# Performance work log

Measured on AMD Instinct MI355X. Metric: run time of the kernel, lower is better.

Reference implementation:

```python
import jax, jax.numpy as jnp
import numpy as np
from jax import lax

BS = 131072
L = 128          # pitch dim (conv input length)
NUM_CH = 10
EMB = 256
Z_DIM = 128
K = 64           # num codebook embeddings
COMMIT = 0.25


def setup_inputs() -> dict:
    key = jax.random.key(0)
    ks = jax.random.split(key, 10)
    pr = jax.random.uniform(ks[0], (BS, L), dtype=jnp.float32)
    track_pad_mask = jax.random.randint(ks[1], (BS,), 0, 2).astype(jnp.bool_)
    conv_w = jax.random.normal(ks[2], (NUM_CH, 1, 12), dtype=jnp.float32) * 0.1
    conv_b = jnp.zeros((NUM_CH,), jnp.float32)
    fc_w = jax.random.normal(ks[3], (EMB, NUM_CH * 29), dtype=jnp.float32) * 0.05
    fc_b = jnp.zeros((EMB,), jnp.float32)
    mu_w = jax.random.normal(ks[4], (Z_DIM, EMB), dtype=jnp.float32) * 0.05
    mu_b = jnp.zeros((Z_DIM,), jnp.float32)
    codebook = jax.random.normal(ks[5], (K, Z_DIM), dtype=jnp.float32)
    return {"pr": pr, "track_pad_mask": track_pad_mask, "conv_w": conv_w,
            "conv_b": conv_b, "fc_w": fc_w, "fc_b": fc_b,
            "mu_w": mu_w, "mu_b": mu_b, "codebook": codebook}


def _encode(pr, conv_w, conv_b, fc_w, fc_b, mu_w, mu_b):
    # Conv1d(1 -> NUM_CH, k=12, stride=1, VALID): [bs,1,128] -> [bs,10,117]
    x = lax.conv_general_dilated(pr[:, None, :], conv_w, (1,), 'VALID',
                                 dimension_numbers=('NCH', 'OIH', 'NCH'))
    x = jax.nn.relu(x + conv_b[None, :, None])
    # MaxPool1d(4,4): [bs,10,117] -> [bs,10,29]
    x = lax.reduce_window(x, -jnp.inf, lax.max, (1, 1, 4), (1, 1, 4), 'VALID')
    x = x.reshape(x.shape[0], -1)               # [bs, 290]
    x = x @ fc_w.T + fc_b                       # [bs, 256]
    mu = x @ mu_w.T + mu_b                      # [bs, 128]
    return mu


def _vq(mu, codebook, track_pad_mask):
    # squared L2 distances [bs, K]
    d = (jnp.sum(mu * mu, axis=1, keepdims=True)
         - 2.0 * mu @ codebook.T
         + jnp.sum(codebook * codebook, axis=1)[None, :])
    idx = jnp.argmin(d, axis=1)                 # [bs]
    q = codebook[idx]                           # gather [bs, Z_DIM]
    valid = (~track_pad_mask).astype(mu.dtype)  # [bs]
    n_valid = jnp.maximum(jnp.sum(valid), 1.0)
    # commitment loss over non-padded rows
    e_latent = jnp.sum(((lax.stop_gradient(q) - mu) ** 2) * valid[:, None]) / (n_valid * mu.shape[1])
    cmt_loss = COMMIT * e_latent
    # straight-through estimator
    z = mu + lax.stop_gradient(q - mu)
    # perplexity over non-padded assignments
    counts = jnp.zeros((K,), mu.dtype).at[idx].add(valid)
    probs = counts / n_valid
    perplexity = jnp.exp(-jnp.sum(probs * jnp.log(probs + 1e-10)))
    return z, cmt_loss, perplexity


def reference(pr, track_pad_mask, conv_w, conv_b, fc_w, fc_b, mu_w, mu_b, codebook):
    mu = _encode(pr, conv_w, conv_b, fc_w, fc_b, mu_w, mu_b)
    z, cmt_loss, perplexity = _vq(mu, codebook, track_pad_mask)
    return z, cmt_loss, perplexity
```

## Files before the change

kernel.cpp:

```cpp
#include <hip/hip_runtime.h>
#include <math.h>

#define BS 131072
#define L 128
#define NCH 10
#define EMB 256
#define ZD 128
#define KCB 64
#define NF 290
#define RPB 64
#define TPB 128

typedef __attribute__((ext_vector_type(8))) short short8;
typedef __attribute__((ext_vector_type(4))) float float4v;

#define WS_BC    0
#define WS_CNORM 128
#define WS_CBT   192
#define WS_CNT   8384
#define WS_ESUM  8448
#define WS_WHI   8452
#define WS_WLO   28932

static __device__ __forceinline__ short f2bf(float x) {
  unsigned u = __float_as_uint(x);
  return (short)((u + 0x7fffu + ((u >> 16) & 1u)) >> 16);
}
static __device__ __forceinline__ float bf2f(short s) {
  return __uint_as_float(((unsigned)(unsigned short)s) << 16);
}

__global__ void k_prep(const float* __restrict__ fc_w, const float* __restrict__ fc_b,
                       const float* __restrict__ mu_w, const float* __restrict__ mu_b,
                       const float* __restrict__ codebook, float* __restrict__ ws) {
  const int b = blockIdx.x, t = threadIdx.x;
  if (b < 80) {
    __shared__ float fcT[32 * 260];
    __shared__ float mus[16 * 260];
    const int c = b >> 4, ks = (b >> 3) & 1, nt = b & 7;
    const int f0 = c * 58 + ks * 32;

    {
      const int kk = t & 31, esub = t >> 5;
      const bool valid = (ks * 32 + kk) < 58;
#pragma unroll
      for (int p = 0; p < 32; ++p) {
        int e = p * 8 + esub;
        fcT[kk * 260 + e] = valid ? fc_w[e * NF + f0 + kk] : 0.0f;
      }
    }
    {
#pragma unroll
      for (int p = 0; p < 4; ++p) {
        int idx = p * 256 + t;
        int zz = idx >> 6, e4 = idx & 63;
        *(float4*)&mus[zz * 260 + e4 * 4] =
            *(const float4*)&mu_w[(nt * 16 + zz) * EMB + e4 * 4];
      }
    }
    __syncthreads();

    const int lane_lo = t >> 3, j = t & 7;
    const int z = lane_lo & 15;
    const int kka = ((lane_lo >> 4) & 1) * 8 + j;
    const int kkb = kka + 16;
    float a0 = 0, a1 = 0, a2 = 0, a3 = 0, b0 = 0, b1 = 0, b2 = 0, b3 = 0;
#pragma unroll 8
    for (int e = 0; e < 256; e += 4) {
      float4 m  = *(const float4*)&mus[z * 260 + e];
      float4 fa = *(const float4*)&fcT[kka * 260 + e];
      float4 fb = *(const float4*)&fcT[kkb * 260 + e];
      a0 = fmaf(m.x, fa.x, a0); a1 = fmaf(m.y, fa.y, a1);
      a2 = fmaf(m.z, fa.z, a2); a3 = fmaf(m.w, fa.w, a3);
      b0 = fmaf(m.x, fb.x, b0); b1 = fmaf(m.y, fb.y, b1);
      b2 = fmaf(m.z, fb.z, b2); b3 = fmaf(m.w, fb.w, b3);
    }
    float va = (a0 + a1) + (a2 + a3);
    float vb = (b0 + b1) + (b2 + b3);
    short* hi = (short*)(ws + WS_WHI);
    short* lo = (short*)(ws + WS_WLO);
    const int base = b * 512;
    short ha = f2bf(va); short la = f2bf(va - bf2f(ha));
    short hb = f2bf(vb); short lb = f2bf(vb - bf2f(hb));
    hi[base + t] = ha;        lo[base + t] = la;
    hi[base + 256 + t] = hb;  lo[base + 256 + t] = lb;
  } else if (b == 80) {
    if (t < ZD) {
      float p0 = 0, p1 = 0, p2 = 0, p3 = 0;
      const float* mw = mu_w + (size_t)t * EMB;
      for (int e = 0; e < EMB; e += 4) {
        p0 = fmaf(mw[e + 0], fc_b[e + 0], p0);
        p1 = fmaf(mw[e + 1], fc_b[e + 1], p1);
        p2 = fmaf(mw[e + 2], fc_b[e + 2], p2);
        p3 = fmaf(mw[e + 3], fc_b[e + 3], p3);
      }
      ws[WS_BC + t] = mu_b[t] + ((p0 + p1) + (p2 + p3));
    }
  } else if (b == 81) {
    if (t < KCB) {
      double acc = 0.0;
      for (int k = 0; k < ZD; ++k) { double v = (double)codebook[t * ZD + k]; acc += v * v; }
      ws[WS_CNORM + t] = (float)acc;
    } else if (t < 128) {
      ((int*)ws)[WS_CNT + (t - 64)] = 0;
    } else if (t == 128) {
      ws[WS_ESUM] = 0.0f;
    }
  } else {
    for (int i = 0; i < 32; ++i) {
      int idx = i * 256 + t;
      int k = idx >> 6, cc = idx & 63;
      ws[WS_CBT + idx] = codebook[cc * ZD + k];
    }
  }
}

__launch_bounds__(TPB, 2)
__global__ void k_main(const float* __restrict__ pr, const int* __restrict__ mask,
                       const float* __restrict__ conv_w, const float* __restrict__ conv_b,
                       const float* __restrict__ codebook,
                       float* __restrict__ ws, float* __restrict__ out) {
  __shared__ __align__(16) unsigned char lds_raw[33024];
  __shared__ float aux_val[RPB * 8];
  __shared__ int   aux_idx[RPB * 8];
  __shared__ int   bi_s[RPB];
  __shared__ float validf[RPB];
  __shared__ int   hist[KCB];

  short* feat_hi = (short*)lds_raw;
  short* feat_lo = (short*)(lds_raw + 9216);
  float* mu_s    = (float*)lds_raw;

  const int tid = threadIdx.x;
  const int lane = tid & 63, wv = tid >> 6;
  const int q4 = lane >> 4, c16 = lane & 15;
  const long rowg0 = (long)blockIdx.x * RPB;

  if (tid < KCB) hist[tid] = 0;
  for (int i = tid; i < RPB * 6; i += TPB) {
    int r = i / 6, kk = 58 + (i % 6);
    feat_hi[r * 72 + kk] = 0;
    feat_lo[r * 72 + kk] = 0;
  }

  const float* bc = ws + WS_BC;
  float4v acc[4][4];
#pragma unroll
  for (int ntl = 0; ntl < 4; ++ntl) {
    float bv = bc[wv * 64 + ntl * 16 + c16];
    float4v b4 = {bv, bv, bv, bv};
#pragma unroll
    for (int mt = 0; mt < 4; ++mt) acc[mt][ntl] = b4;
  }

  const short* whi = (const short*)(ws + WS_WHI);
  const short* wlo = (const short*)(ws + WS_WLO);

  const int cr = tid >> 1, hh = tid & 1;
  const float* prow = pr + (rowg0 + cr) * (long)L;
  const int j0 = hh * 15, njj = 15 - hh;

#pragma unroll 1
  for (int ck = 0; ck < 5; ++ck) {
#pragma unroll 1
    for (int chl = 0; chl < 2; ++chl) {
      const int ch = ck * 2 + chl;
      float w[12];
#pragma unroll
      for (int u = 0; u < 12; ++u) w[u] = conv_w[ch * 12 + u];
      const float cbias = conv_b[ch];

      float wb[20];
      *(float4*)&wb[0]  = *(const float4*)&prow[4 * j0];
      *(float4*)&wb[4]  = *(const float4*)&prow[4 * j0 + 4];
      *(float4*)&wb[8]  = *(const float4*)&prow[4 * j0 + 8];
      *(float4*)&wb[12] = *(const float4*)&prow[4 * j0 + 12];
#pragma unroll
      for (int jj = 0; jj < 15; ++jj) {
        if (jj < njj) {
          int j = j0 + jj;
          if (jj + 1 < njj)
            *(float4*)&wb[((jj + 4) % 5) * 4] = *(const float4*)&prow[4 * j + 16];
          float m4 = -1e30f;
#pragma unroll
          for (int d = 0; d < 4; ++d) {
            float a = cbias;
#pragma unroll
            for (int u = 0; u < 12; ++u) a = fmaf(w[u], wb[(4 * jj + d + u) % 20], a);
            m4 = fmaxf(m4, a);
          }
          float v = fmaxf(m4, 0.0f);
          int kl = chl * 29 + j;
          short h = f2bf(v);
          feat_hi[cr * 72 + kl] = h;
          feat_lo[cr * 72 + kl] = f2bf(v - bf2f(h));
        }
      }
    }
    __syncthreads();

#pragma unroll
    for (int ks = 0; ks < 2; ++ks) {
      short8 ah[4], al[4];
#pragma unroll
      for (int mt = 0; mt < 4; ++mt) {
        int off = (mt * 16 + c16) * 72 + ks * 32 + q4 * 8;
        ah[mt] = *(const short8*)(feat_hi + off);
        al[mt] = *(const short8*)(feat_lo + off);
      }
#pragma unroll
      for (int ntl = 0; ntl < 4; ++ntl) {
        int nt = wv * 4 + ntl;
        int fo = (((ck * 2 + ks) * 8 + nt) * 64 + lane) * 8;
        short8 bh = *(const short8*)(whi + fo);
        short8 bl = *(const short8*)(wlo + fo);
#pragma unroll
        for (int mt = 0; mt < 4; ++mt) {
          acc[mt][ntl] = __builtin_amdgcn_mfma_f32_16x16x32_bf16(ah[mt], bh, acc[mt][ntl], 0, 0, 0);
          acc[mt][ntl] = __builtin_amdgcn_mfma_f32_16x16x32_bf16(ah[mt], bl, acc[mt][ntl], 0, 0, 0);
          acc[mt][ntl] = __builtin_amdgcn_mfma_f32_16x16x32_bf16(al[mt], bh, acc[mt][ntl], 0, 0, 0);
        }
      }
    }
    __syncthreads();
  }

#pragma unroll
  for (int mt = 0; mt < 4; ++mt)
#pragma unroll
    for (int ntl = 0; ntl < 4; ++ntl) {
      int col = wv * 64 + ntl * 16 + c16;
      int rowb = mt * 16 + q4 * 4;
#pragma unroll
      for (int r = 0; r < 4; ++r)
        mu_s[(rowb + r) * 129 + col] = acc[mt][ntl][r];
    }
  __syncthreads();

  const float* cnorm = ws + WS_CNORM;
  const float* cbT   = ws + WS_CBT;
  const int tvr = tid & 15, tvc = tid >> 4;
  const int rv0 = tvr * 4, cbo = tvc * 8;
  float s[4][8];
#pragma unroll
  for (int i = 0; i < 4; ++i)
#pragma unroll
    for (int j = 0; j < 8; ++j) s[i][j] = 0.0f;
#pragma unroll 4
  for (int k = 0; k < 128; ++k) {
    float m0 = mu_s[(rv0 + 0) * 129 + k];
    float m1 = mu_s[(rv0 + 1) * 129 + k];
    float m2 = mu_s[(rv0 + 2) * 129 + k];
    float m3 = mu_s[(rv0 + 3) * 129 + k];
    float4 ca = *(const float4*)&cbT[k * 64 + cbo];
    float4 cb4 = *(const float4*)&cbT[k * 64 + cbo + 4];
    float cv[8] = {ca.x, ca.y, ca.z, ca.w, cb4.x, cb4.y, cb4.z, cb4.w};
    float mv[4] = {m0, m1, m2, m3};
#pragma unroll
    for (int i = 0; i < 4; ++i)
#pragma unroll
      for (int j = 0; j < 8; ++j) s[i][j] = fmaf(mv[i], cv[j], s[i][j]);
  }
  {
    float4 n0 = *(const float4*)&cnorm[cbo];
    float4 n1 = *(const float4*)&cnorm[cbo + 4];
    float nv[8] = {n0.x, n0.y, n0.z, n0.w, n1.x, n1.y, n1.z, n1.w};
#pragma unroll
    for (int i = 0; i < 4; ++i) {
      float best = nv[0] - 2.0f * s[i][0];
      int bi = cbo;
#pragma unroll
      for (int j = 1; j < 8; ++j) {
        float d = nv[j] - 2.0f * s[i][j];
        if (d < best) { best = d; bi = cbo + j; }
      }
      aux_val[(rv0 + i) * 8 + tvc] = best;
      aux_idx[(rv0 + i) * 8 + tvc] = bi;
    }
  }
  __syncthreads();

  if (tid < RPB) {
    float best = aux_val[tid * 8];
    int bi = aux_idx[tid * 8];
#pragma unroll
    for (int v = 1; v < 8; ++v) {
      float x = aux_val[tid * 8 + v];
      if (x < best) { best = x; bi = aux_idx[tid * 8 + v]; }
    }
    bi_s[tid] = bi;
    validf[tid] = (mask[rowg0 + tid] == 0) ? 1.0f : 0.0f;
  }
  __syncthreads();
  if (tid < RPB) {
    if (validf[tid] > 0.5f) atomicAdd(&hist[bi_s[tid]], 1);
  }
  __syncthreads();
  if (tid < KCB && hist[tid] > 0) atomicAdd(&((int*)ws)[WS_CNT + tid], hist[tid]);

  float eloc = 0.0f;
  float* zout = out + rowg0 * ZD;
#pragma unroll 2
  for (int p = 0; p < RPB; ++p) {
    int bi = bi_s[p];
    float q = codebook[bi * ZD + tid];
    float m = mu_s[p * 129 + tid];
    zout[(size_t)p * ZD + tid] = q;
    float d = q - m;
    eloc += validf[p] * d * d;
  }
#pragma unroll
  for (int o = 32; o > 0; o >>= 1) eloc += __shfl_xor(eloc, o, 64);
  if ((tid & 63) == 0) atomicAdd(&ws[WS_ESUM], eloc);
}

__global__ void k_final(const float* __restrict__ ws, float* __restrict__ out) {
  int t = threadIdx.x;
  const int* cnt = (const int*)ws + WS_CNT;
  double c = (double)cnt[t];
  double nv = c;
#pragma unroll
  for (int o = 32; o > 0; o >>= 1) nv += __shfl_xor(nv, o, 64);
  nv = fmax(nv, 1.0);
  double p = c / nv;
  double h = p * log(p + 1e-10);
#pragma unroll
  for (int o = 32; o > 0; o >>= 1) h += __shfl_xor(h, o, 64);
  if (t == 0) {
    out[(size_t)BS * ZD]     = (float)(0.25 * (double)ws[WS_ESUM] / (nv * 128.0));
    out[(size_t)BS * ZD + 1] = (float)exp(-h);
  }
}

extern "C" void kernel_launch(void* const* d_in, const int* in_sizes, int n_in,
                              void* d_out, int out_size, void* d_ws, size_t ws_size,
                              hipStream_t stream) {
  const float* pr      = (const float*)d_in[0];
  const int*   mask    = (const int*)d_in[1];
  const float* conv_w  = (const float*)d_in[2];
  const float* conv_b  = (const float*)d_in[3];
  const float* fc_w    = (const float*)d_in[4];
  const float* fc_b    = (const float*)d_in[5];
  const float* mu_w    = (const float*)d_in[6];
  const float* mu_b    = (const float*)d_in[7];
  const float* codebook= (const float*)d_in[8];
  float* ws  = (float*)d_ws;
  float* out = (float*)d_out;

  hipLaunchKernelGGL(k_prep, dim3(83), dim3(256), 0, stream,
                     fc_w, fc_b, mu_w, mu_b, codebook, ws);
  hipLaunchKernelGGL(k_main, dim3(BS / RPB), dim3(TPB), 0, stream,
                     pr, mask, conv_w, conv_b, codebook, ws, out);
  hipLaunchKernelGGL(k_final, dim3(1), dim3(64), 0, stream, ws, out);
}
```

Baseline: 295.3 us.

## Compute Conv1d on MFMA via bf16 split and restructure encoder per 16-row group

Replaces the scalar FMA Conv1d+maxpool with MFMA bf16x3 (hi/lo split) matmuls against a Toeplitz-packed conv weight held in registers. Input rows are staged into LDS as bf16 hi/lo. The encoder is reorganized to process 16-row groups with all 290 features at once, so the fused FC weight layout in prep is changed to a contiguous K layout. The aim is to move the dominant conv FLOPs off the VALU onto matrix cores. The cost is extra MFMA work from zero-padded channels and Toeplitz padding, plus possible precision differences from the 3-term bf16 emulation.

```diff
diff --git a/kernel.cpp b/kernel.cpp
--- a/kernel.cpp
+++ b/kernel.cpp
@@ -11,7 +11,11 @@
 #define RPB 64
 #define TPB 128
 
+#define FP 296
+#define PP 164
+
 typedef __attribute__((ext_vector_type(8))) short short8;
+typedef __attribute__((ext_vector_type(4))) short short4v;
 typedef __attribute__((ext_vector_type(4))) float float4v;
 
 #define WS_BC    0
@@ -29,6 +33,14 @@
 static __device__ __forceinline__ float bf2f(short s) {
   return __uint_as_float(((unsigned)(unsigned short)s) << 16);
 }
+static __device__ __forceinline__ short8 ld_b64x2(const short* p) {
+  short4v a = *(const short4v*)p;
+  short4v b = *(const short4v*)(p + 4);
+  short8 r;
+  r[0]=a[0]; r[1]=a[1]; r[2]=a[2]; r[3]=a[3];
+  r[4]=b[0]; r[5]=b[1]; r[6]=b[2]; r[7]=b[3];
+  return r;
+}
 
 __global__ void k_prep(const float* __restrict__ fc_w, const float* __restrict__ fc_b,
                        const float* __restrict__ mu_w, const float* __restrict__ mu_b,
@@ -37,12 +49,13 @@
   if (b < 80) {
     __shared__ float fcT[32 * 260];
     __shared__ float mus[16 * 260];
-    const int c = b >> 4, ks = (b >> 3) & 1, nt = b & 7;
-    const int f0 = c * 58 + ks * 32;
+    const int ks = b >> 3, nt = b & 7;
+    const int f0 = ks * 32;
+    const int nval = (290 - f0 < 32) ? (290 - f0) : 32;
 
     {
       const int kk = t & 31, esub = t >> 5;
-      const bool valid = (ks * 32 + kk) < 58;
+      const bool valid = kk < nval;
 #pragma unroll
       for (int p = 0; p < 32; ++p) {
         int e = p * 8 + esub;
@@ -128,7 +141,9 @@
   __shared__ int   hist[KCB];
 
   short* feat_hi = (short*)lds_raw;
-  short* feat_lo = (short*)(lds_raw + 9216);
+  short* feat_lo = (short*)(lds_raw + 9472);
+  short* prs_hi  = (short*)(lds_raw + 18944);
+  short* prs_lo  = (short*)(lds_raw + 24192);
   float* mu_s    = (float*)lds_raw;
 
   const int tid = threadIdx.x;
@@ -137,10 +152,38 @@
   const long rowg0 = (long)blockIdx.x * RPB;
 
   if (tid < KCB) hist[tid] = 0;
-  for (int i = tid; i < RPB * 6; i += TPB) {
-    int r = i / 6, kk = 58 + (i % 6);
-    feat_hi[r * 72 + kk] = 0;
-    feat_lo[r * 72 + kk] = 0;
+  for (int i = tid; i < 16 * 6; i += TPB) {
+    int r = i / 6, kk = 290 + (i % 6);
+    feat_hi[r * FP + kk] = 0;
+    feat_lo[r * FP + kk] = 0;
+  }
+  for (int i = tid; i < 16 * 36; i += TPB) {
+    int r = i / 36, kk = 128 + (i % 36);
+    prs_hi[r * PP + kk] = 0;
+    prs_lo[r * PP + kk] = 0;
+  }
+
+  short8 cwh[3], cwl[3];
+  {
+    const int chl = c16 >> 2, d = c16 & 3;
+#pragma unroll
+    for (int cg = 0; cg < 3; ++cg) {
+      const int ch = cg * 4 + chl;
+#pragma unroll
+      for (int e = 0; e < 8; ++e) {
+        int v = q4 * 8 + e, u = v - d;
+        float val = (ch < NCH && u >= 0 && u < 12) ? conv_w[ch * 12 + u] : 0.0f;
+        short h = f2bf(val);
+        cwh[cg][e] = h;
+        cwl[cg][e] = f2bf(val - bf2f(h));
+      }
+    }
+  }
+  float cb[3];
+#pragma unroll
+  for (int cg = 0; cg < 3; ++cg) {
+    int ch = cg * 4 + q4;
+    cb[cg] = (ch < NCH) ? conv_b[ch] : 0.0f;
   }
 
   const float* bc = ws + WS_BC;
@@ -150,90 +193,87 @@
     float bv = bc[wv * 64 + ntl * 16 + c16];
     float4v b4 = {bv, bv, bv, bv};
 #pragma unroll
-    for (int mt = 0; mt < 4; ++mt) acc[mt][ntl] = b4;
+    for (int rg = 0; rg < 4; ++rg) acc[rg][ntl] = b4;
   }
 
   const short* whi = (const short*)(ws + WS_WHI);
   const short* wlo = (const short*)(ws + WS_WLO);
 
-  const int cr = tid >> 1, hh = tid & 1;
-  const float* prow = pr + (rowg0 + cr) * (long)L;
-  const int j0 = hh * 15, njj = 15 - hh;
+  const int jlo = wv * 15;
+  const int jhi = wv ? 29 : 15;
+  const int srow = tid >> 3, sseg = tid & 7;
+
+#pragma unroll
+  for (int rg = 0; rg < 4; ++rg) {
+    {
+      const float* pg = pr + (rowg0 + rg * 16 + srow) * (long)L + sseg * 16;
+      short* ph = prs_hi + srow * PP + sseg * 16;
+      short* pl = prs_lo + srow * PP + sseg * 16;
+#pragma unroll
+      for (int i = 0; i < 4; ++i) {
+        float4 v = *(const float4*)(pg + i * 4);
+        short h0 = f2bf(v.x), h1 = f2bf(v.y), h2 = f2bf(v.z), h3 = f2bf(v.w);
+        short4v hv = {h0, h1, h2, h3};
+        short4v lv = {f2bf(v.x - bf2f(h0)), f2bf(v.y - bf2f(h1)),
+                      f2bf(v.z - bf2f(h2)), f2bf(v.w - bf2f(h3))};
+        *(short4v*)(ph + i * 4) = hv;
+        *(short4v*)(pl + i * 4) = lv;
+      }
+    }
+    __syncthreads();
 
 #pragma unroll 1
-  for (int ck = 0; ck < 5; ++ck) {
-#pragma unroll 1
-    for (int chl = 0; chl < 2; ++chl) {
-      const int ch = ck * 2 + chl;
-      float w[12];
-#pragma unroll
-      for (int u = 0; u < 12; ++u) w[u] = conv_w[ch * 12 + u];
-      const float cbias = conv_b[ch];
-
-      float wb[20];
-      *(float4*)&wb[0]  = *(const float4*)&prow[4 * j0];
-      *(float4*)&wb[4]  = *(const float4*)&prow[4 * j0 + 4];
-      *(float4*)&wb[8]  = *(const float4*)&prow[4 * j0 + 8];
-      *(float4*)&wb[12] = *(const float4*)&prow[4 * j0 + 12];
-#pragma unroll
-      for (int jj = 0; jj < 15; ++jj) {
-        if (jj < njj) {
-          int j = j0 + jj;
-          if (jj + 1 < njj)
-            *(float4*)&wb[((jj + 4) % 5) * 4] = *(const float4*)&prow[4 * j + 16];
-          float m4 = -1e30f;
-#pragma unroll
-          for (int d = 0; d < 4; ++d) {
-            float a = cbias;
-#pragma unroll
-            for (int u = 0; u < 12; ++u) a = fmaf(w[u], wb[(4 * jj + d + u) % 20], a);
-            m4 = fmaxf(m4, a);
-          }
-          float v = fmaxf(m4, 0.0f);
-          int kl = chl * 29 + j;
-          short h = f2bf(v);
-          feat_hi[cr * 72 + kl] = h;
-          feat_lo[cr * 72 + kl] = f2bf(v - bf2f(h));
+    for (int j = jlo; j < jhi; ++j) {
+      const int po = c16 * PP + 4 * j + 8 * q4;
+      short8 bh = ld_b64x2(prs_hi + po);
+      short8 bl = ld_b64x2(prs_lo + po);
+#pragma unroll
+      for (int cg = 0; cg < 3; ++cg) {
+        float bv = cb[cg];
+        float4v c = {bv, bv, bv, bv};
+        c = __builtin_amdgcn_mfma_f32_16x16x32_bf16(cwh[cg], bh, c, 0, 0, 0);
+        c = __builtin_amdgcn_mfma_f32_16x16x32_bf16(cwh[cg], bl, c, 0, 0, 0);
+        c = __builtin_amdgcn_mfma_f32_16x16x32_bf16(cwl[cg], bh, c, 0, 0, 0);
+        if (cg < 2 || q4 < 2) {
+          float m = fmaxf(fmaxf(c[0], c[1]), fmaxf(c[2], c[3]));
+          m = fmaxf(m, 0.0f);
+          int kl = (cg * 4 + q4) * 29 + j;
+          short h = f2bf(m);
+          feat_hi[c16 * FP + kl] = h;
+          feat_lo[c16 * FP + kl] = f2bf(m - bf2f(h));
         }
       }
     }
     __syncthreads();
 
-#pragma unroll
-    for (int ks = 0; ks < 2; ++ks) {
-      short8 ah[4], al[4];
-#pragma unroll
-      for (int mt = 0; mt < 4; ++mt) {
-        int off = (mt * 16 + c16) * 72 + ks * 32 + q4 * 8;
-        ah[mt] = *(const short8*)(feat_hi + off);
-        al[mt] = *(const short8*)(feat_lo + off);
-      }
+#pragma unroll 2
+    for (int g = 0; g < 10; ++g) {
+      const int ao = c16 * FP + g * 32 + q4 * 8;
+      short8 ah = *(const short8*)(feat_hi + ao);
+      short8 al = *(const short8*)(feat_lo + ao);
 #pragma unroll
       for (int ntl = 0; ntl < 4; ++ntl) {
         int nt = wv * 4 + ntl;
-        int fo = (((ck * 2 + ks) * 8 + nt) * 64 + lane) * 8;
+        int fo = ((g * 8 + nt) * 64 + lane) * 8;
         short8 bh = *(const short8*)(whi + fo);
         short8 bl = *(const short8*)(wlo + fo);
-#pragma unroll
-        for (int mt = 0; mt < 4; ++mt) {
-          acc[mt][ntl] = __builtin_amdgcn_mfma_f32_16x16x32_bf16(ah[mt], bh, acc[mt][ntl], 0, 0, 0);
-          acc[mt][ntl] = __builtin_amdgcn_mfma_f32_16x16x32_bf16(ah[mt], bl, acc[mt][ntl], 0, 0, 0);
-          acc[mt][ntl] = __builtin_amdgcn_mfma_f32_16x16x32_bf16(al[mt], bh, acc[mt][ntl], 0, 0, 0);
-        }
+        acc[rg][ntl] = __builtin_amdgcn_mfma_f32_16x16x32_bf16(ah, bh, acc[rg][ntl], 0, 0, 0);
+        acc[rg][ntl] = __builtin_amdgcn_mfma_f32_16x16x32_bf16(ah, bl, acc[rg][ntl], 0, 0, 0);
+        acc[rg][ntl] = __builtin_amdgcn_mfma_f32_16x16x32_bf16(al, bh, acc[rg][ntl], 0, 0, 0);
       }
     }
     __syncthreads();
   }
 
 #pragma unroll
-  for (int mt = 0; mt < 4; ++mt)
+  for (int rg = 0; rg < 4; ++rg)
 #pragma unroll
     for (int ntl = 0; ntl < 4; ++ntl) {
       int col = wv * 64 + ntl * 16 + c16;
-      int rowb = mt * 16 + q4 * 4;
+      int rowb = rg * 16 + q4 * 4;
 #pragma unroll
       for (int r = 0; r < 4; ++r)
-        mu_s[(rowb + r) * 129 + col] = acc[mt][ntl][r];
+        mu_s[(rowb + r) * 129 + col] = acc[rg][ntl][r];
     }
   __syncthreads();
 
```

Result: slower. 319.6 us (+8.2%).

## Halve LDS footprint via two-phase VQ epilogue and fuse conv channel pairs

Applied to the files above, without the earlier changes.

The mu tile is now staged to shared memory in two 32-row halves. Each half runs its own distance, argmin, histogram and output pass, which shrinks the LDS buffer from about 33KB to 18KB. Launch bounds go from 2 to 4 blocks per SM so more waves can be resident. The conv loop computes two channels per pass over the same input window, so prow is loaded once per channel pair. The cost is extra barriers, smaller per-thread distance tiles, and register pressure from the tighter launch bound, which may cause spills given the 16 float4 MFMA accumulators.

```diff
diff --git a/kernel.cpp b/kernel.cpp
--- a/kernel.cpp
+++ b/kernel.cpp
@@ -115,16 +115,16 @@
   }
 }
 
-__launch_bounds__(TPB, 2)
+__launch_bounds__(TPB, 4)
 __global__ void k_main(const float* __restrict__ pr, const int* __restrict__ mask,
                        const float* __restrict__ conv_w, const float* __restrict__ conv_b,
                        const float* __restrict__ codebook,
                        float* __restrict__ ws, float* __restrict__ out) {
-  __shared__ __align__(16) unsigned char lds_raw[33024];
-  __shared__ float aux_val[RPB * 8];
-  __shared__ int   aux_idx[RPB * 8];
-  __shared__ int   bi_s[RPB];
-  __shared__ float validf[RPB];
+  __shared__ __align__(16) unsigned char lds_raw[18432];
+  __shared__ float aux_val[32 * 16];
+  __shared__ int   aux_idx[32 * 16];
+  __shared__ int   bi_s[32];
+  __shared__ float validf[32];
   __shared__ int   hist[KCB];
 
   short* feat_hi = (short*)lds_raw;
@@ -162,13 +162,15 @@
 
 #pragma unroll 1
   for (int ck = 0; ck < 5; ++ck) {
-#pragma unroll 1
-    for (int chl = 0; chl < 2; ++chl) {
-      const int ch = ck * 2 + chl;
-      float w[12];
-#pragma unroll
-      for (int u = 0; u < 12; ++u) w[u] = conv_w[ch * 12 + u];
-      const float cbias = conv_b[ch];
+    {
+      const int ch0 = ck * 2;
+      float w0[12], w1[12];
+#pragma unroll
+      for (int u = 0; u < 12; ++u) {
+        w0[u] = conv_w[ch0 * 12 + u];
+        w1[u] = conv_w[ch0 * 12 + 12 + u];
+      }
+      const float cb0 = conv_b[ch0], cb1 = conv_b[ch0 + 1];
 
       float wb[20];
       *(float4*)&wb[0]  = *(const float4*)&prow[4 * j0];
@@ -181,19 +183,27 @@
           int j = j0 + jj;
           if (jj + 1 < njj)
             *(float4*)&wb[((jj + 4) % 5) * 4] = *(const float4*)&prow[4 * j + 16];
-          float m4 = -1e30f;
+          float m40 = -1e30f, m41 = -1e30f;
 #pragma unroll
           for (int d = 0; d < 4; ++d) {
-            float a = cbias;
-#pragma unroll
-            for (int u = 0; u < 12; ++u) a = fmaf(w[u], wb[(4 * jj + d + u) % 20], a);
-            m4 = fmaxf(m4, a);
+            float a0 = cb0, a1 = cb1;
+#pragma unroll
+            for (int u = 0; u < 12; ++u) {
+              float x = wb[(4 * jj + d + u) % 20];
+              a0 = fmaf(w0[u], x, a0);
+              a1 = fmaf(w1[u], x, a1);
+            }
+            m40 = fmaxf(m40, a0);
+            m41 = fmaxf(m41, a1);
           }
-          float v = fmaxf(m4, 0.0f);
-          int kl = chl * 29 + j;
-          short h = f2bf(v);
-          feat_hi[cr * 72 + kl] = h;
-          feat_lo[cr * 72 + kl] = f2bf(v - bf2f(h));
+          float v0 = fmaxf(m40, 0.0f);
+          float v1 = fmaxf(m41, 0.0f);
+          short h0 = f2bf(v0);
+          feat_hi[cr * 72 + j] = h0;
+          feat_lo[cr * 72 + j] = f2bf(v0 - bf2f(h0));
+          short h1 = f2bf(v1);
+          feat_hi[cr * 72 + 29 + j] = h1;
+          feat_lo[cr * 72 + 29 + j] = f2bf(v1 - bf2f(h1));
         }
       }
     }
@@ -225,90 +235,93 @@
     __syncthreads();
   }
 
-#pragma unroll
-  for (int mt = 0; mt < 4; ++mt)
-#pragma unroll
-    for (int ntl = 0; ntl < 4; ++ntl) {
-      int col = wv * 64 + ntl * 16 + c16;
-      int rowb = mt * 16 + q4 * 4;
-#pragma unroll
-      for (int r = 0; r < 4; ++r)
-        mu_s[(rowb + r) * 129 + col] = acc[mt][ntl][r];
-    }
-  __syncthreads();
-
   const float* cnorm = ws + WS_CNORM;
   const float* cbT   = ws + WS_CBT;
-  const int tvr = tid & 15, tvc = tid >> 4;
-  const int rv0 = tvr * 4, cbo = tvc * 8;
-  float s[4][8];
-#pragma unroll
-  for (int i = 0; i < 4; ++i)
-#pragma unroll
-    for (int j = 0; j < 8; ++j) s[i][j] = 0.0f;
+  const int tvr = tid & 7, tvc = tid >> 3;
+  const int lr0 = tvr * 4, cbo = tvc * 4;
+  float eloc = 0.0f;
+
+#pragma unroll
+  for (int ph = 0; ph < 2; ++ph) {
+#pragma unroll
+    for (int mh = 0; mh < 2; ++mh) {
+      const int mt = ph * 2 + mh;
+#pragma unroll
+      for (int ntl = 0; ntl < 4; ++ntl) {
+        int col = wv * 64 + ntl * 16 + c16;
+        int rowb = mh * 16 + q4 * 4;
+#pragma unroll
+        for (int r = 0; r < 4; ++r)
+          mu_s[(rowb + r) * 129 + col] = acc[mt][ntl][r];
+      }
+    }
+    __syncthreads();
+
+    float s[4][4];
+#pragma unroll
+    for (int i = 0; i < 4; ++i)
+#pragma unroll
+      for (int j = 0; j < 4; ++j) s[i][j] = 0.0f;
 #pragma unroll 4
-  for (int k = 0; k < 128; ++k) {
-    float m0 = mu_s[(rv0 + 0) * 129 + k];
-    float m1 = mu_s[(rv0 + 1) * 129 + k];
-    float m2 = mu_s[(rv0 + 2) * 129 + k];
-    float m3 = mu_s[(rv0 + 3) * 129 + k];
-    float4 ca = *(const float4*)&cbT[k * 64 + cbo];
-    float4 cb4 = *(const float4*)&cbT[k * 64 + cbo + 4];
-    float cv[8] = {ca.x, ca.y, ca.z, ca.w, cb4.x, cb4.y, cb4.z, cb4.w};
-    float mv[4] = {m0, m1, m2, m3};
-#pragma unroll
-    for (int i = 0; i < 4; ++i)
-#pragma unroll
-      for (int j = 0; j < 8; ++j) s[i][j] = fmaf(mv[i], cv[j], s[i][j]);
-  }
-  {
-    float4 n0 = *(const float4*)&cnorm[cbo];
-    float4 n1 = *(const float4*)&cnorm[cbo + 4];
-    float nv[8] = {n0.x, n0.y, n0.z, n0.w, n1.x, n1.y, n1.z, n1.w};
-#pragma unroll
-    for (int i = 0; i < 4; ++i) {
-      float best = nv[0] - 2.0f * s[i][0];
-      int bi = cbo;
-#pragma unroll
-      for (int j = 1; j < 8; ++j) {
-        float d = nv[j] - 2.0f * s[i][j];
-        if (d < best) { best = d; bi = cbo + j; }
-      }
-      aux_val[(rv0 + i) * 8 + tvc] = best;
-      aux_idx[(rv0 + i) * 8 + tvc] = bi;
-    }
-  }
-  __syncthreads();
-
-  if (tid < RPB) {
-    float best = aux_val[tid * 8];
-    int bi = aux_idx[tid * 8];
-#pragma unroll
-    for (int v = 1; v < 8; ++v) {
-      float x = aux_val[tid * 8 + v];
-      if (x < best) { best = x; bi = aux_idx[tid * 8 + v]; }
-    }
-    bi_s[tid] = bi;
-    validf[tid] = (mask[rowg0 + tid] == 0) ? 1.0f : 0.0f;
-  }
-  __syncthreads();
-  if (tid < RPB) {
-    if (validf[tid] > 0.5f) atomicAdd(&hist[bi_s[tid]], 1);
-  }
-  __syncthreads();
+    for (int k = 0; k < 128; ++k) {
+      float m0 = mu_s[(lr0 + 0) * 129 + k];
+      float m1 = mu_s[(lr0 + 1) * 129 + k];
+      float m2 = mu_s[(lr0 + 2) * 129 + k];
+      float m3 = mu_s[(lr0 + 3) * 129 + k];
+      float4 cv = *(const float4*)&cbT[k * 64 + cbo];
+      float c4[4] = {cv.x, cv.y, cv.z, cv.w};
+      float mv[4] = {m0, m1, m2, m3};
+#pragma unroll
+      for (int i = 0; i < 4; ++i)
+#pragma unroll
+        for (int j = 0; j < 4; ++j) s[i][j] = fmaf(mv[i], c4[j], s[i][j]);
+    }
+    {
+      float4 n = *(const float4*)&cnorm[cbo];
+      float nv[4] = {n.x, n.y, n.z, n.w};
+#pragma unroll
+      for (int i = 0; i < 4; ++i) {
+        float best = nv[0] - 2.0f * s[i][0];
+        int bi = cbo;
+#pragma unroll
+        for (int j = 1; j < 4; ++j) {
+          float d = nv[j] - 2.0f * s[i][j];
+          if (d < best) { best = d; bi = cbo + j; }
+        }
+        aux_val[(lr0 + i) * 16 + tvc] = best;
+        aux_idx[(lr0 + i) * 16 + tvc] = bi;
+      }
+    }
+    __syncthreads();
+
+    if (tid < 32) {
+      float best = aux_val[tid * 16];
+      int bi = aux_idx[tid * 16];
+#pragma unroll
+      for (int v = 1; v < 16; ++v) {
+        float x = aux_val[tid * 16 + v];
+        if (x < best) { best = x; bi = aux_idx[tid * 16 + v]; }
+      }
+      bi_s[tid] = bi;
+      validf[tid] = (mask[rowg0 + ph * 32 + tid] == 0) ? 1.0f : 0.0f;
+    }
+    __syncthreads();
+    if (tid < 32 && validf[tid] > 0.5f) atomicAdd(&hist[bi_s[tid]], 1);
+
+    float* zo = out + (rowg0 + ph * 32) * ZD;
+#pragma unroll 2
+    for (int p = 0; p < 32; ++p) {
+      int bi = bi_s[p];
+      float q = codebook[bi * ZD + tid];
+      float m = mu_s[p * 129 + tid];
+      zo[(size_t)p * ZD + tid] = q;
+      float d = q - m;
+      eloc += validf[p] * d * d;
+    }
+    __syncthreads();
+  }
+
   if (tid < KCB && hist[tid] > 0) atomicAdd(&((int*)ws)[WS_CNT + tid], hist[tid]);
-
-  float eloc = 0.0f;
-  float* zout = out + rowg0 * ZD;
-#pragma unroll 2
-  for (int p = 0; p < RPB; ++p) {
-    int bi = bi_s[p];
-    float q = codebook[bi * ZD + tid];
-    float m = mu_s[p * 129 + tid];
-    zout[(size_t)p * ZD + tid] = q;
-    float d = q - m;
-    eloc += validf[p] * d * d;
-  }
 #pragma unroll
   for (int o = 32; o > 0; o >>= 1) eloc += __shfl_xor(eloc, o, 64);
   if ((tid & 63) == 0) atomicAdd(&ws[WS_ESUM], eloc);
```

Measured after the change: 460.6 us. 1.56x slower.

## Fuse conv channel pair, prefetch MFMA weights, vectorize mu LDS reads

Applied to the files above, without the earlier changes.

Each thread now computes both conv channels in a single pass, so every input element loaded serves two accumulators. The first prow window is loaded once and hoisted out of the channel loop. The first k-slice's bf16 weight fragments are prefetched before the conv work, so those global loads overlap with it. The mu tile pitch becomes 132 so the distance loop can read mu with float4 LDS loads, and the output loop is unrolled further. The cost is higher register pressure under launch bounds (128,2) and a different LDS bank-conflict pattern.

```diff
diff --git a/kernel.cpp b/kernel.cpp
--- a/kernel.cpp
+++ b/kernel.cpp
@@ -10,6 +10,8 @@
 #define NF 290
 #define RPB 64
 #define TPB 128
+
+#define MUP 132
 
 typedef __attribute__((ext_vector_type(8))) short short8;
 typedef __attribute__((ext_vector_type(4))) float float4v;
@@ -120,7 +122,7 @@
                        const float* __restrict__ conv_w, const float* __restrict__ conv_b,
                        const float* __restrict__ codebook,
                        float* __restrict__ ws, float* __restrict__ out) {
-  __shared__ __align__(16) unsigned char lds_raw[33024];
+  __shared__ __align__(16) unsigned char lds_raw[33792];
   __shared__ float aux_val[RPB * 8];
   __shared__ int   aux_idx[RPB * 8];
   __shared__ int   bi_s[RPB];
@@ -160,58 +162,99 @@
   const float* prow = pr + (rowg0 + cr) * (long)L;
   const int j0 = hh * 15, njj = 15 - hh;
 
+  const float4 wbi0 = *(const float4*)&prow[4 * j0];
+  const float4 wbi1 = *(const float4*)&prow[4 * j0 + 4];
+  const float4 wbi2 = *(const float4*)&prow[4 * j0 + 8];
+  const float4 wbi3 = *(const float4*)&prow[4 * j0 + 12];
+
 #pragma unroll 1
   for (int ck = 0; ck < 5; ++ck) {
-#pragma unroll 1
-    for (int chl = 0; chl < 2; ++chl) {
-      const int ch = ck * 2 + chl;
-      float w[12];
-#pragma unroll
-      for (int u = 0; u < 12; ++u) w[u] = conv_w[ch * 12 + u];
-      const float cbias = conv_b[ch];
+    short8 pbh[4], pbl[4];
+#pragma unroll
+    for (int ntl = 0; ntl < 4; ++ntl) {
+      int nt = wv * 4 + ntl;
+      int fo = (((ck * 2 + 0) * 8 + nt) * 64 + lane) * 8;
+      pbh[ntl] = *(const short8*)(whi + fo);
+      pbl[ntl] = *(const short8*)(wlo + fo);
+    }
+
+    {
+      const int ch0 = ck * 2;
+      float w0[12], w1[12];
+#pragma unroll
+      for (int u = 0; u < 12; ++u) {
+        w0[u] = conv_w[ch0 * 12 + u];
+        w1[u] = conv_w[ch0 * 12 + 12 + u];
+      }
+      const float cb0 = conv_b[ch0], cb1 = conv_b[ch0 + 1];
 
       float wb[20];
-      *(float4*)&wb[0]  = *(const float4*)&prow[4 * j0];
-      *(float4*)&wb[4]  = *(const float4*)&prow[4 * j0 + 4];
-      *(float4*)&wb[8]  = *(const float4*)&prow[4 * j0 + 8];
-      *(float4*)&wb[12] = *(const float4*)&prow[4 * j0 + 12];
+      *(float4*)&wb[0]  = wbi0;
+      *(float4*)&wb[4]  = wbi1;
+      *(float4*)&wb[8]  = wbi2;
+      *(float4*)&wb[12] = wbi3;
 #pragma unroll
       for (int jj = 0; jj < 15; ++jj) {
         if (jj < njj) {
           int j = j0 + jj;
           if (jj + 1 < njj)
             *(float4*)&wb[((jj + 4) % 5) * 4] = *(const float4*)&prow[4 * j + 16];
-          float m4 = -1e30f;
+          float m40 = -1e30f, m41 = -1e30f;
 #pragma unroll
           for (int d = 0; d < 4; ++d) {
-            float a = cbias;
-#pragma unroll
-            for (int u = 0; u < 12; ++u) a = fmaf(w[u], wb[(4 * jj + d + u) % 20], a);
-            m4 = fmaxf(m4, a);
+            float a0 = cb0, a1 = cb1;
+#pragma unroll
+            for (int u = 0; u < 12; ++u) {
+              float x = wb[(4 * jj + d + u) % 20];
+              a0 = fmaf(w0[u], x, a0);
+              a1 = fmaf(w1[u], x, a1);
+            }
+            m40 = fmaxf(m40, a0);
+            m41 = fmaxf(m41, a1);
           }
-          float v = fmaxf(m4, 0.0f);
-          int kl = chl * 29 + j;
-          short h = f2bf(v);
-          feat_hi[cr * 72 + kl] = h;
-          feat_lo[cr * 72 + kl] = f2bf(v - bf2f(h));
+          float v0 = fmaxf(m40, 0.0f);
+          float v1 = fmaxf(m41, 0.0f);
+          short h0 = f2bf(v0);
+          feat_hi[cr * 72 + j] = h0;
+          feat_lo[cr * 72 + j] = f2bf(v0 - bf2f(h0));
+          short h1 = f2bf(v1);
+          feat_hi[cr * 72 + 29 + j] = h1;
+          feat_lo[cr * 72 + 29 + j] = f2bf(v1 - bf2f(h1));
         }
       }
     }
     __syncthreads();
 
-#pragma unroll
-    for (int ks = 0; ks < 2; ++ks) {
+    {
       short8 ah[4], al[4];
 #pragma unroll
       for (int mt = 0; mt < 4; ++mt) {
-        int off = (mt * 16 + c16) * 72 + ks * 32 + q4 * 8;
+        int off = (mt * 16 + c16) * 72 + q4 * 8;
         ah[mt] = *(const short8*)(feat_hi + off);
         al[mt] = *(const short8*)(feat_lo + off);
       }
 #pragma unroll
       for (int ntl = 0; ntl < 4; ++ntl) {
+#pragma unroll
+        for (int mt = 0; mt < 4; ++mt) {
+          acc[mt][ntl] = __builtin_amdgcn_mfma_f32_16x16x32_bf16(ah[mt], pbh[ntl], acc[mt][ntl], 0, 0, 0);
+          acc[mt][ntl] = __builtin_amdgcn_mfma_f32_16x16x32_bf16(ah[mt], pbl[ntl], acc[mt][ntl], 0, 0, 0);
+          acc[mt][ntl] = __builtin_amdgcn_mfma_f32_16x16x32_bf16(al[mt], pbh[ntl], acc[mt][ntl], 0, 0, 0);
+        }
+      }
+    }
+    {
+      short8 ah[4], al[4];
+#pragma unroll
+      for (int mt = 0; mt < 4; ++mt) {
+        int off = (mt * 16 + c16) * 72 + 32 + q4 * 8;
+        ah[mt] = *(const short8*)(feat_hi + off);
+        al[mt] = *(const short8*)(feat_lo + off);
+      }
+#pragma unroll
+      for (int ntl = 0; ntl < 4; ++ntl) {
         int nt = wv * 4 + ntl;
-        int fo = (((ck * 2 + ks) * 8 + nt) * 64 + lane) * 8;
+        int fo = (((ck * 2 + 1) * 8 + nt) * 64 + lane) * 8;
         short8 bh = *(const short8*)(whi + fo);
         short8 bl = *(const short8*)(wlo + fo);
 #pragma unroll
@@ -233,7 +276,7 @@
       int rowb = mt * 16 + q4 * 4;
 #pragma unroll
       for (int r = 0; r < 4; ++r)
-        mu_s[(rowb + r) * 129 + col] = acc[mt][ntl][r];
+        mu_s[(rowb + r) * MUP + col] = acc[mt][ntl][r];
     }
   __syncthreads();
 
@@ -246,20 +289,25 @@
   for (int i = 0; i < 4; ++i)
 #pragma unroll
     for (int j = 0; j < 8; ++j) s[i][j] = 0.0f;
-#pragma unroll 4
-  for (int k = 0; k < 128; ++k) {
-    float m0 = mu_s[(rv0 + 0) * 129 + k];
-    float m1 = mu_s[(rv0 + 1) * 129 + k];
-    float m2 = mu_s[(rv0 + 2) * 129 + k];
-    float m3 = mu_s[(rv0 + 3) * 129 + k];
-    float4 ca = *(const float4*)&cbT[k * 64 + cbo];
-    float4 cb4 = *(const float4*)&cbT[k * 64 + cbo + 4];
-    float cv[8] = {ca.x, ca.y, ca.z, ca.w, cb4.x, cb4.y, cb4.z, cb4.w};
-    float mv[4] = {m0, m1, m2, m3};
-#pragma unroll
-    for (int i = 0; i < 4; ++i)
-#pragma unroll
-      for (int j = 0; j < 8; ++j) s[i][j] = fmaf(mv[i], cv[j], s[i][j]);
+#pragma unroll 2
+  for (int k4 = 0; k4 < 128; k4 += 4) {
+    float4 mr0 = *(const float4*)&mu_s[(rv0 + 0) * MUP + k4];
+    float4 mr1 = *(const float4*)&mu_s[(rv0 + 1) * MUP + k4];
+    float4 mr2 = *(const float4*)&mu_s[(rv0 + 2) * MUP + k4];
+    float4 mr3 = *(const float4*)&mu_s[(rv0 + 3) * MUP + k4];
+#pragma unroll
+    for (int kk = 0; kk < 4; ++kk) {
+      int k = k4 + kk;
+      float4 ca = *(const float4*)&cbT[k * 64 + cbo];
+      float4 cb4 = *(const float4*)&cbT[k * 64 + cbo + 4];
+      float cv[8] = {ca.x, ca.y, ca.z, ca.w, cb4.x, cb4.y, cb4.z, cb4.w};
+      float mv[4] = {((const float*)&mr0)[kk], ((const float*)&mr1)[kk],
+                     ((const float*)&mr2)[kk], ((const float*)&mr3)[kk]};
+#pragma unroll
+      for (int i = 0; i < 4; ++i)
+#pragma unroll
+        for (int j = 0; j < 8; ++j) s[i][j] = fmaf(mv[i], cv[j], s[i][j]);
+    }
   }
   {
     float4 n0 = *(const float4*)&cnorm[cbo];
@@ -300,11 +348,11 @@
 
   float eloc = 0.0f;
   float* zout = out + rowg0 * ZD;
-#pragma unroll 2
+#pragma unroll 8
   for (int p = 0; p < RPB; ++p) {
     int bi = bi_s[p];
     float q = codebook[bi * ZD + tid];
-    float m = mu_s[p * 129 + tid];
+    float m = mu_s[p * MUP + tid];
     zout[(size_t)p * ZD + tid] = q;
     float d = q - m;
     eloc += validf[p] * d * d;
```

Measured after the change: 301.6 us. 2.1% more time.
